# Optimization experiments

Measured on AMD Instinct MI355X. Metric: run time of the kernel, lower is better.

The kernel has to match this reference:

```python
import jax, jax.numpy as jnp
import numpy as np

EPS = 1e-9

def _quaternion_normalize(q):
    # normalize last dim with eps for stability
    return q / jnp.sqrt(jnp.sum(q * q, axis=-1, keepdims=True) + EPS)

def setup_inputs() -> dict:
    key = jax.random.key(0)
    k1, k2 = jax.random.split(key)
    # byte trajectory values in [0, 255), float so they carry gradients
    starcoder_bytes = jax.random.uniform(k1, (4096,), dtype=jnp.float32) * 255.0
    # DNA indices 0:A 1:C 2:G 3:T
    hg38_indices = jax.random.randint(k2, (4096,), 0, 4)
    return {"starcoder_bytes": starcoder_bytes, "hg38_indices": hg38_indices}

def _gauss_linking(r1, r2):
    # discrete Gauss linking integral over segment midpoints
    dr1 = r1[1:] - r1[:-1]              # [N-1, 3] segment tangents
    dr2 = r2[1:] - r2[:-1]              # [M-1, 3]
    m1 = 0.5 * (r1[1:] + r1[:-1])       # [N-1, 3] midpoints
    m2 = 0.5 * (r2[1:] + r2[:-1])       # [M-1, 3]
    diff = m1[:, None, :] - m2[None, :, :]            # [N-1, M-1, 3]
    cr = jnp.cross(dr1[:, None, :], dr2[None, :, :])  # [N-1, M-1, 3]
    num = jnp.sum(cr * diff, axis=-1)                 # [N-1, M-1]
    dist2 = jnp.sum(diff * diff, axis=-1) + EPS
    return jnp.sum(num * dist2 ** -1.5) / (4.0 * jnp.pi)

def reference(starcoder_bytes, hg38_indices):
    # map_bytes_to_quaternion
    theta = starcoder_bytes / 255.0 * (2.0 * jnp.pi)
    c, s = jnp.cos(theta), jnp.sin(theta)
    q_algo = _quaternion_normalize(
        jnp.stack([c, 0.5 * s, 0.3 * s, 0.2 * s], axis=-1))  # [N, 4]
    # map_fasta_to_quaternion (one-hot basis, already unit norm)
    basis = jnp.eye(4, dtype=jnp.float32)
    q_bio = _quaternion_normalize(basis[hg38_indices])        # [M, 4]
    # imaginary parts -> 3D trajectories
    r1 = q_algo[:, 1:]
    r2 = q_bio[:, 1:]
    lk = _gauss_linking(r1, r2)
    return lk
```

## Files before the change

kernel.cpp:

```cpp
#include <hip/hip_runtime.h>
#include <math.h>

#define N 4096
#define M 4095
#define EPSF 1e-9f
#define NT 1024
#define INV_4PI 0.07957747154594767f

__global__ __launch_bounds__(NT) void fused_gauss_kernel(
    const float* __restrict__ bytes, const int* __restrict__ idx,
    float* __restrict__ out) {
  __shared__ float r1x[N], r1y[N], r1z[N];
  __shared__ int hist[16];
  __shared__ float wsum[NT / 64];

  const int tid = threadIdx.x;
  if (tid < 16) hist[tid] = 0;
  __syncthreads();

#pragma unroll
  for (int k = 0; k < N / NT; ++k) {
    int i = tid + k * NT;
    float rev = bytes[i] * (1.0f / 255.0f);
    float s = __builtin_amdgcn_sinf(rev);
    float c = __builtin_amdgcn_cosf(rev);
    float q1 = 0.5f * s, q2 = 0.3f * s, q3 = 0.2f * s;
    float n2 = c * c + q1 * q1 + q2 * q2 + q3 * q3 + EPSF;
    float inv = rsqrtf(n2);
    inv = inv * (1.5f - 0.5f * n2 * inv * inv);
    r1x[i] = q1 * inv;
    r1y[i] = q2 * inv;
    r1z[i] = q3 * inv;
    int a = idx[i];
    if (i < M) {
      int b = idx[i + 1];
      if (a != b) atomicAdd(&hist[a * 4 + b], 1);
    }
  }
  __syncthreads();

  const float PX[4] = {0.f, 1.f, 0.f, 0.f};
  const float PY[4] = {0.f, 0.f, 1.f, 0.f};
  const float PZ[4] = {0.f, 0.f, 0.f, 1.f};
  const int TA[6] = {0, 0, 0, 1, 1, 2};
  const int TB[6] = {1, 2, 3, 2, 3, 3};
  float w[6];
#pragma unroll
  for (int t = 0; t < 6; ++t)
    w[t] = (float)(hist[TA[t] * 4 + TB[t]] - hist[TB[t] * 4 + TA[t]]);

  float acc = 0.0f;
#pragma unroll
  for (int k = 0; k < N / NT; ++k) {
    int i = tid + k * NT;
    if (i < M) {
      float ax = r1x[i], ay = r1y[i], az = r1z[i];
      float bx = r1x[i + 1], by = r1y[i + 1], bz = r1z[i + 1];
      float d1x = bx - ax, d1y = by - ay, d1z = bz - az;
      float m1x = 0.5f * (bx + ax), m1y = 0.5f * (by + ay), m1z = 0.5f * (bz + az);

#pragma unroll
      for (int t = 0; t < 6; ++t) {
        const int a = TA[t], b = TB[t];
        const float ex = PX[b] - PX[a];
        const float ey = PY[b] - PY[a];
        const float ez = PZ[b] - PZ[a];
        const float m2x = 0.5f * (PX[a] + PX[b]);
        const float m2y = 0.5f * (PY[a] + PY[b]);
        const float m2z = 0.5f * (PZ[a] + PZ[b]);

        float dx = m1x - m2x, dy = m1y - m2y, dz = m1z - m2z;
        float cx = d1y * ez - d1z * ey;
        float cy = d1z * ex - d1x * ez;
        float cz = d1x * ey - d1y * ex;
        float num = cx * dx + cy * dy + cz * dz;
        float d2 = dx * dx + dy * dy + dz * dz + EPSF;
        float inv = rsqrtf(d2);
        inv = inv * (1.5f - 0.5f * d2 * inv * inv);
        acc += w[t] * num * (inv * inv * inv);
      }
    }
  }

  for (int off = 32; off > 0; off >>= 1)
    acc += __shfl_down(acc, off, 64);
  int lane = tid & 63, wid = tid >> 6;
  if (lane == 0) wsum[wid] = acc;
  __syncthreads();
  if (tid == 0) {
    float t = 0.0f;
#pragma unroll
    for (int wv = 0; wv < NT / 64; ++wv) t += wsum[wv];
    out[0] = t * INV_4PI;
  }
}

extern "C" void kernel_launch(void* const* d_in, const int* in_sizes, int n_in,
                              void* d_out, int out_size, void* d_ws, size_t ws_size,
                              hipStream_t stream) {
  const float* bytes = (const float*)d_in[0];
  const int* idx = (const int*)d_in[1];
  float* out = (float*)d_out;

  fused_gauss_kernel<<<dim3(1), dim3(NT), 0, stream>>>(bytes, idx, out);
}
```

Measured before the change: 60.12 us.

## Replace shared-memory histogram and staging with per-thread registers and shuffle reductions

Each thread now loads four contiguous bytes and indices with vector loads, plus one neighbour element, and keeps the trajectory points in registers. This removes the shared-memory staging arrays. The transition histogram built with shared atomics is replaced by per-thread signed counts for the six edge types, and the geometric sums for those six edges are accumulated separately. Both sets of twelve partial sums are reduced with wave shuffles and a small shared table, then combined as a dot product at the end. This drops atomic contention and one barrier phase, at the cost of twelve shuffle reductions instead of one.

```diff
diff --git a/kernel.cpp b/kernel.cpp
--- a/kernel.cpp
+++ b/kernel.cpp
@@ -10,88 +10,102 @@
 __global__ __launch_bounds__(NT) void fused_gauss_kernel(
     const float* __restrict__ bytes, const int* __restrict__ idx,
     float* __restrict__ out) {
-  __shared__ float r1x[N], r1y[N], r1z[N];
-  __shared__ int hist[16];
-  __shared__ float wsum[NT / 64];
+  __shared__ float red[NT / 64][12];
+  __shared__ float fin[12];
 
-  const int tid = threadIdx.x;
-  if (tid < 16) hist[tid] = 0;
-  __syncthreads();
+  const int t = threadIdx.x;
 
+  const float4 b4 = reinterpret_cast<const float4*>(bytes)[t];
+  const int4 i4 = reinterpret_cast<const int4*>(idx)[t];
+  const bool last = (t == NT - 1);
+  const float b5 = last ? 0.0f : bytes[4 * t + 4];
+  const int i5 = last ? 0 : idx[4 * t + 4];
+
+  const float bb[5] = {b4.x, b4.y, b4.z, b4.w, b5};
+  const int ii[5] = {i4.x, i4.y, i4.z, i4.w, i5};
+
+  float px[5], py[5], pz[5];
 #pragma unroll
-  for (int k = 0; k < N / NT; ++k) {
-    int i = tid + k * NT;
-    float rev = bytes[i] * (1.0f / 255.0f);
+  for (int k = 0; k < 5; ++k) {
+    float rev = bb[k] * (1.0f / 255.0f);
     float s = __builtin_amdgcn_sinf(rev);
     float c = __builtin_amdgcn_cosf(rev);
     float q1 = 0.5f * s, q2 = 0.3f * s, q3 = 0.2f * s;
     float n2 = c * c + q1 * q1 + q2 * q2 + q3 * q3 + EPSF;
     float inv = rsqrtf(n2);
     inv = inv * (1.5f - 0.5f * n2 * inv * inv);
-    r1x[i] = q1 * inv;
-    r1y[i] = q2 * inv;
-    r1z[i] = q3 * inv;
-    int a = idx[i];
-    if (i < M) {
-      int b = idx[i + 1];
-      if (a != b) atomicAdd(&hist[a * 4 + b], 1);
+    px[k] = q1 * inv;
+    py[k] = q2 * inv;
+    pz[k] = q3 * inv;
+  }
+
+  const float EX[6] = {1.f, 0.f, 0.f, -1.f, -1.f, 0.f};
+  const float EY[6] = {0.f, 1.f, 0.f, 1.f, 0.f, -1.f};
+  const float EZ[6] = {0.f, 0.f, 1.f, 0.f, 1.f, 1.f};
+  const float M2X[6] = {0.5f, 0.f, 0.f, 0.5f, 0.5f, 0.f};
+  const float M2Y[6] = {0.f, 0.5f, 0.f, 0.5f, 0.f, 0.5f};
+  const float M2Z[6] = {0.f, 0.f, 0.5f, 0.f, 0.5f, 0.5f};
+  const int AB[6] = {0 * 4 + 1, 0 * 4 + 2, 0 * 4 + 3, 1 * 4 + 2, 1 * 4 + 3, 2 * 4 + 3};
+  const int BA[6] = {1 * 4 + 0, 2 * 4 + 0, 3 * 4 + 0, 2 * 4 + 1, 3 * 4 + 1, 3 * 4 + 2};
+
+  float S[6] = {0.f, 0.f, 0.f, 0.f, 0.f, 0.f};
+  float W[6] = {0.f, 0.f, 0.f, 0.f, 0.f, 0.f};
+
+#pragma unroll
+  for (int k = 0; k < 4; ++k) {
+    if (4 * t + k < M) {
+      float ax = px[k], ay = py[k], az = pz[k];
+      float bx = px[k + 1], by = py[k + 1], bz = pz[k + 1];
+      float d1x = bx - ax, d1y = by - ay, d1z = bz - az;
+      float m1x = 0.5f * (bx + ax), m1y = 0.5f * (by + ay), m1z = 0.5f * (bz + az);
+      int u = ii[k] * 4 + ii[k + 1];
+
+#pragma unroll
+      for (int q = 0; q < 6; ++q) {
+        float dx = m1x - M2X[q], dy = m1y - M2Y[q], dz = m1z - M2Z[q];
+        float cx = d1y * EZ[q] - d1z * EY[q];
+        float cy = d1z * EX[q] - d1x * EZ[q];
+        float cz = d1x * EY[q] - d1y * EX[q];
+        float num = cx * dx + cy * dy + cz * dz;
+        float d2 = dx * dx + dy * dy + dz * dz + EPSF;
+        float inv = rsqrtf(d2);
+        inv = inv * (1.5f - 0.5f * d2 * inv * inv);
+        S[q] += num * (inv * inv * inv);
+        W[q] += (u == AB[q] ? 1.0f : 0.0f) - (u == BA[q] ? 1.0f : 0.0f);
+      }
+    }
+  }
+
+#pragma unroll
+  for (int off = 32; off > 0; off >>= 1) {
+#pragma unroll
+    for (int q = 0; q < 6; ++q) {
+      S[q] += __shfl_down(S[q], off, 64);
+      W[q] += __shfl_down(W[q], off, 64);
+    }
+  }
+  const int lane = t & 63, wid = t >> 6;
+  if (lane == 0) {
+#pragma unroll
+    for (int q = 0; q < 6; ++q) {
+      red[wid][q] = S[q];
+      red[wid][q + 6] = W[q];
     }
   }
   __syncthreads();
 
-  const float PX[4] = {0.f, 1.f, 0.f, 0.f};
-  const float PY[4] = {0.f, 0.f, 1.f, 0.f};
-  const float PZ[4] = {0.f, 0.f, 0.f, 1.f};
-  const int TA[6] = {0, 0, 0, 1, 1, 2};
-  const int TB[6] = {1, 2, 3, 2, 3, 3};
-  float w[6];
+  if (t < 12) {
+    float v = 0.0f;
 #pragma unroll
-  for (int t = 0; t < 6; ++t)
-    w[t] = (float)(hist[TA[t] * 4 + TB[t]] - hist[TB[t] * 4 + TA[t]]);
-
-  float acc = 0.0f;
+    for (int w = 0; w < NT / 64; ++w) v += red[w][t];
+    fin[t] = v;
+  }
+  __syncthreads();
+  if (t == 0) {
+    float r = 0.0f;
 #pragma unroll
-  for (int k = 0; k < N / NT; ++k) {
-    int i = tid + k * NT;
-    if (i < M) {
-      float ax = r1x[i], ay = r1y[i], az = r1z[i];
-      float bx = r1x[i + 1], by = r1y[i + 1], bz = r1z[i + 1];
-      float d1x = bx - ax, d1y = by - ay, d1z = bz - az;
-      float m1x = 0.5f * (bx + ax), m1y = 0.5f * (by + ay), m1z = 0.5f * (bz + az);
-
-#pragma unroll
-      for (int t = 0; t < 6; ++t) {
-        const int a = TA[t], b = TB[t];
-        const float ex = PX[b] - PX[a];
-        const float ey = PY[b] - PY[a];
-        const float ez = PZ[b] - PZ[a];
-        const float m2x = 0.5f * (PX[a] + PX[b]);
-        const float m2y = 0.5f * (PY[a] + PY[b]);
-        const float m2z = 0.5f * (PZ[a] + PZ[b]);
-
-        float dx = m1x - m2x, dy = m1y - m2y, dz = m1z - m2z;
-        float cx = d1y * ez - d1z * ey;
-        float cy = d1z * ex - d1x * ez;
-        float cz = d1x * ey - d1y * ex;
-        float num = cx * dx + cy * dy + cz * dz;
-        float d2 = dx * dx + dy * dy + dz * dz + EPSF;
-        float inv = rsqrtf(d2);
-        inv = inv * (1.5f - 0.5f * d2 * inv * inv);
-        acc += w[t] * num * (inv * inv * inv);
-      }
-    }
-  }
-
-  for (int off = 32; off > 0; off >>= 1)
-    acc += __shfl_down(acc, off, 64);
-  int lane = tid & 63, wid = tid >> 6;
-  if (lane == 0) wsum[wid] = acc;
-  __syncthreads();
-  if (tid == 0) {
-    float t = 0.0f;
-#pragma unroll
-    for (int wv = 0; wv < NT / 64; ++wv) t += wsum[wv];
-    out[0] = t * INV_4PI;
+    for (int q = 0; q < 6; ++q) r += fin[q + 6] * fin[q];
+    out[0] = r * INV_4PI;
   }
 }
 
```

Measured after the change: 60.03 us. No clear change (-0.2%).
